# Kernel optimization log

Hardware: AMD Instinct MI355X
Metric: run time of the kernel (lower is better)

## Reference

```python
import jax, jax.numpy as jnp
import numpy as np

DIM = 128
EDGE_FEAT_DIM = 2
N_NODES = 50000
N_EDGES = 600000
EPS = 1e-5


def setup_inputs() -> dict:
    key = jax.random.key(0)
    ks = jax.random.split(key, 16)
    d = DIM
    inp = {}
    inp["x"] = jax.random.normal(ks[0], (N_NODES, d), dtype=jnp.float32)
    inp["edge_index"] = jax.random.randint(ks[1], (2, N_EDGES), 0, N_NODES, dtype=jnp.int32)
    inp["edge_weight_norm"] = jax.random.uniform(ks[2], (N_EDGES,), dtype=jnp.float32)
    inp["edge_feat"] = jax.random.normal(ks[3], (N_EDGES, EDGE_FEAT_DIM), dtype=jnp.float32)
    inp["batch"] = jnp.zeros((N_NODES,), dtype=jnp.int32)
    # phi: Linear(dim, dim)
    inp["W_phi"] = jax.random.normal(ks[4], (d, d), dtype=jnp.float32) * (1.0 / np.sqrt(d))
    inp["b_phi"] = jnp.zeros((d,), dtype=jnp.float32)
    # edge_gate: Linear(2d+2, d) -> BN(d) -> GELU -> Linear(d, 1)
    din = 2 * d + EDGE_FEAT_DIM
    inp["W_g1"] = jax.random.normal(ks[5], (din, d), dtype=jnp.float32) * (1.0 / np.sqrt(din))
    inp["b_g1"] = jnp.zeros((d,), dtype=jnp.float32)
    inp["bn_gamma"] = jnp.ones((d,), dtype=jnp.float32)
    inp["bn_beta"] = jnp.zeros((d,), dtype=jnp.float32)
    inp["bn_mean"] = jnp.zeros((d,), dtype=jnp.float32)
    inp["bn_var"] = jnp.ones((d,), dtype=jnp.float32)
    inp["W_g2"] = jax.random.normal(ks[6], (d, 1), dtype=jnp.float32) * (1.0 / np.sqrt(d))
    inp["b_g2"] = jnp.zeros((1,), dtype=jnp.float32)
    # upd: Linear(2d, d)
    inp["W_u"] = jax.random.normal(ks[7], (2 * d, d), dtype=jnp.float32) * (1.0 / np.sqrt(2 * d))
    inp["b_u"] = jnp.zeros((d,), dtype=jnp.float32)
    # LayerNorm(dim)
    inp["ln_gamma"] = jnp.ones((d,), dtype=jnp.float32)
    inp["ln_beta"] = jnp.zeros((d,), dtype=jnp.float32)
    return inp


def reference(x, edge_index, edge_weight_norm, edge_feat, batch,
              W_phi, b_phi, W_g1, b_g1, bn_gamma, bn_beta, bn_mean, bn_var,
              W_g2, b_g2, W_u, b_u, ln_gamma, ln_beta):
    src, dst = edge_index[0], edge_index[1]
    # phi(x): [N, d]
    xj = x @ W_phi + b_phi
    # edge gate MLP on [x_dst, x_src, e]: [E, 2d+2]
    g_in = jnp.concatenate([x[dst], x[src], edge_feat], axis=-1)
    h1 = g_in @ W_g1 + b_g1
    h1 = (h1 - bn_mean) * jax.lax.rsqrt(bn_var + EPS) * bn_gamma + bn_beta  # BN eval mode
    h1 = jax.nn.gelu(h1, approximate=False)
    gate = jax.nn.sigmoid(h1 @ W_g2 + b_g2)[:, 0]  # [E]
    # messages and scatter-add aggregation
    msg = xj[src] * (edge_weight_norm * gate)[:, None]  # [E, d]
    agg = jax.ops.segment_sum(msg, dst, num_segments=x.shape[0])  # [N, d]
    # update MLP + GELU + residual + LayerNorm
    h = jnp.concatenate([x, agg], axis=-1) @ W_u + b_u
    h = jax.nn.gelu(h, approximate=False)
    y = x + h
    mu = jnp.mean(y, axis=-1, keepdims=True)
    var = jnp.var(y, axis=-1, keepdims=True)
    return (y - mu) * jax.lax.rsqrt(var + EPS) * ln_gamma + ln_beta
```

## Files before the change

### kernel.cpp

```cpp
#include <hip/hip_runtime.h>
#include <hip/hip_fp16.h>
#include <math.h>

#define DIM 128
#define NN 50000
#define NE 600000
#define EPS 1e-5f
#define CAP 64

struct H8 { __half2 h[4]; };
struct F8 { float4 a, b; };

typedef _Float16 f16x8 __attribute__((ext_vector_type(8)));
typedef float    f32x4 __attribute__((ext_vector_type(4)));

__device__ __forceinline__ float gelu_fast(float x) {
    const float c1 = 2.3022085f;
    const float c2 = 0.1029437f;
    const float x2 = x * x;
    const float z  = x * __builtin_fmaf(c2, x2, c1);
    const float u  = __builtin_amdgcn_exp2f(z);
    const float r  = __builtin_amdgcn_rcpf(1.f + u);
    return __builtin_fmaf(-x, r, x);
}

__device__ __forceinline__ float sigmoid_fast(float y) {
    const float u = __builtin_amdgcn_exp2f(-1.4426950409f * y);
    return __builtin_amdgcn_rcpf(1.f + u);
}

__global__ __launch_bounds__(256) void k_prep_scale(
    const float* __restrict__ Wg1, const float* __restrict__ bg1,
    const float* __restrict__ bng, const float* __restrict__ bnb,
    const float* __restrict__ bnm, const float* __restrict__ bnv,
    __half* __restrict__ WABth, float* __restrict__ bA,
    float* __restrict__ w0p, float* __restrict__ w1p)
{
    const int k = blockIdx.x;
    const int t = threadIdx.x;
    const int c = t & 127;
    const float s = bng[c] * rsqrtf(bnv[c] + EPS);
    const float w = (t < 128) ? Wg1[k * DIM + c] : Wg1[(DIM + k) * DIM + c];
    WABth[t * DIM + k] = __float2half(w * s);
    if (k == 0 && t < 128) {
        const float tt = bnb[c] - bnm[c] * s;
        bA[c]  = bg1[c] * s + tt;
        w0p[c] = Wg1[256 * DIM + c] * s;
        w1p[c] = Wg1[257 * DIM + c] * s;
    }
}

__global__ __launch_bounds__(128) void k_prep_wpu(
    const float* __restrict__ Wphi, const float* __restrict__ bphi,
    const float* __restrict__ Wu,
    __half* __restrict__ Wct, float* __restrict__ bpu)
{
    const int a = blockIdx.x;
    const int j = threadIdx.x;
    float acc = 0.f;
    #pragma unroll 8
    for (int k = 0; k < DIM; ++k)
        acc += Wphi[a * DIM + k] * Wu[(DIM + k) * DIM + j];
    Wct[j * 256 + a]       = __float2half(Wu[a * DIM + j]);
    Wct[j * 256 + 128 + a] = __float2half(acc);
    if (a == 0) {
        float b = 0.f;
        #pragma unroll 8
        for (int k = 0; k < DIM; ++k)
            b += bphi[k] * Wu[(DIM + k) * DIM + j];
        bpu[j] = b;
    }
}

__global__ __launch_bounds__(256) void k_xh(
    const float* __restrict__ x, __half* __restrict__ xh)
{
    const int i = blockIdx.x * 256 + threadIdx.x;
    const float4 v = ((const float4*)x)[i];
    __half2 a, b;
    a.x = __float2half_rn(v.x); a.y = __float2half_rn(v.y);
    b.x = __float2half_rn(v.z); b.y = __float2half_rn(v.w);
    ((__half2*)xh)[2 * i]     = a;
    ((__half2*)xh)[2 * i + 1] = b;
}

__global__ __launch_bounds__(256) void k_node_mfma(
    const __half* __restrict__ xh, const __half* __restrict__ WABth,
    const float* __restrict__ bA,
    __half* __restrict__ A, __half* __restrict__ Bv)
{
    __shared__ __half tile[64][264];
    const int t    = threadIdx.x;
    const int wv   = t >> 6;
    const int lane = t & 63;
    const int n16  = lane & 15;
    const int quad = lane >> 4;
    const int m0   = blockIdx.x * 64;

    f32x4 acc[4][4];
    #pragma unroll
    for (int mt = 0; mt < 4; ++mt)
        #pragma unroll
        for (int nt = 0; nt < 4; ++nt)
            acc[mt][nt] = (f32x4){0.f, 0.f, 0.f, 0.f};

    int rowm[4];
    #pragma unroll
    for (int mt = 0; mt < 4; ++mt)
        rowm[mt] = min(m0 + mt * 16 + n16, NN - 1);

    #pragma unroll
    for (int ks = 0; ks < 4; ++ks) {
        const int ko = ks * 32 + quad * 8;
        f16x8 bf[4];
        #pragma unroll
        for (int nt = 0; nt < 4; ++nt) {
            const int c = wv * 64 + nt * 16 + n16;
            bf[nt] = *(const f16x8*)(WABth + c * DIM + ko);
        }
        #pragma unroll
        for (int mt = 0; mt < 4; ++mt) {
            const f16x8 af = *(const f16x8*)(xh + (size_t)rowm[mt] * DIM + ko);
            #pragma unroll
            for (int nt = 0; nt < 4; ++nt)
                acc[mt][nt] = __builtin_amdgcn_mfma_f32_16x16x32_f16(
                    af, bf[nt], acc[mt][nt], 0, 0, 0);
        }
    }

    #pragma unroll
    for (int nt = 0; nt < 4; ++nt) {
        const int c = wv * 64 + nt * 16 + n16;
        const float bias = (c < 128) ? bA[c] : 0.f;
        #pragma unroll
        for (int mt = 0; mt < 4; ++mt)
            #pragma unroll
            for (int reg = 0; reg < 4; ++reg)
                tile[mt * 16 + quad * 4 + reg][c] =
                    __float2half(acc[mt][nt][reg] + bias);
    }
    __syncthreads();

    #pragma unroll
    for (int i = 0; i < 8; ++i) {
        const int chunk = t + i * 256;
        const int row = chunk >> 5;
        const int o   = (chunk & 31) * 8;
        if (m0 + row < NN) {
            const uint4 v = *(const uint4*)&tile[row][o];
            if (o < 128) *(uint4*)(A  + (size_t)(m0 + row) * DIM + o)       = v;
            else         *(uint4*)(Bv + (size_t)(m0 + row) * DIM + o - 128) = v;
        }
    }
}

__global__ __launch_bounds__(256) void k_gate(
    const int*   __restrict__ ei,  const float* __restrict__ ew,
    const float* __restrict__ ef,
    const __half* __restrict__ A,  const __half* __restrict__ Bv,
    const float* __restrict__ w0p, const float* __restrict__ w1p,
    const float* __restrict__ Wg2, const float* __restrict__ bg2,
    int* __restrict__ deg, int2* __restrict__ pairs)
{
    const int t    = threadIdx.x;
    const int lane = t & 63;
    const int sub  = lane >> 4;
    const int sl   = lane & 15;
    const int c8   = sl * 8;
    const int e    = (blockIdx.x * 4 + (t >> 6)) * 4 + sub;

    const F8 WG = *(const F8*)(Wg2 + c8);
    const F8 W0 = *(const F8*)(w0p + c8);
    const F8 W1 = *(const F8*)(w1p + c8);
    const float bg2v = bg2[0];

    const int src = ei[e];
    const int dst = ei[NE + e];
    const float ef0 = ef[2 * e], ef1 = ef[2 * e + 1];

    const H8 av = *(const H8*)(A  + (size_t)dst * DIM + c8);
    const H8 bv = *(const H8*)(Bv + (size_t)src * DIM + c8);

    float hv[8];
    #pragma unroll
    for (int i = 0; i < 4; ++i) {
        const float2 af = __half22float2(av.h[i]);
        const float2 bf = __half22float2(bv.h[i]);
        hv[2 * i]     = af.x + bf.x;
        hv[2 * i + 1] = af.y + bf.y;
    }
    const float* w0 = (const float*)&W0;
    const float* w1 = (const float*)&W1;
    const float* wg = (const float*)&WG;
    float p = 0.f;
    #pragma unroll
    for (int i = 0; i < 8; ++i) {
        float h = hv[i] + ef0 * w0[i] + ef1 * w1[i];
        p = __builtin_fmaf(gelu_fast(h), wg[i], p);
    }
    #pragma unroll
    for (int off = 1; off < 16; off <<= 1) p += __shfl_xor(p, off, 64);

    if (sl == 0) {
        const float coef = ew[e] * sigmoid_fast(p + bg2v);
        const int pos = atomicAdd(&deg[dst], 1);
        if (pos < CAP)
            pairs[dst * CAP + pos] = make_int2(src, __float_as_int(coef));
    }
}

__global__ __launch_bounds__(256) void k_agg(
    const int* __restrict__ deg, const int2* __restrict__ pairs,
    const __half* __restrict__ xh,
    __half* __restrict__ aggh, float* __restrict__ sc)
{
    const int t    = threadIdx.x;
    const int lane = t & 63;
    const int sub  = lane >> 4;
    const int sl   = lane & 15;
    const int c8   = sl * 8;
    const int n    = blockIdx.x * 4 + (t >> 6);
    const int d    = min(deg[n], CAP);

    float acc[8];
    #pragma unroll
    for (int i = 0; i < 8; ++i) acc[i] = 0.f;
    float scn = 0.f;

    for (int j = sub; j < d; j += 4) {
        const int2 pr = pairs[n * CAP + j];
        const float cf = __int_as_float(pr.y);
        const H8 xv = *(const H8*)(xh + (size_t)pr.x * DIM + c8);
        #pragma unroll
        for (int i = 0; i < 4; ++i) {
            const float2 xf = __half22float2(xv.h[i]);
            acc[2 * i]     = __builtin_fmaf(cf, xf.x, acc[2 * i]);
            acc[2 * i + 1] = __builtin_fmaf(cf, xf.y, acc[2 * i + 1]);
        }
        scn += cf;
    }

    #pragma unroll
    for (int off = 16; off < 64; off <<= 1) {
        #pragma unroll
        for (int i = 0; i < 8; ++i) acc[i] += __shfl_xor(acc[i], off, 64);
        scn += __shfl_xor(scn, off, 64);
    }

    if (sub == 0) {
        H8 hv;
        #pragma unroll
        for (int i = 0; i < 4; ++i) {
            hv.h[i].x = __float2half_rn(acc[2 * i]);
            hv.h[i].y = __float2half_rn(acc[2 * i + 1]);
        }
        *(H8*)(aggh + (size_t)n * DIM + c8) = hv;
        if (sl == 0) sc[n] = scn;
    }
}

__global__ __launch_bounds__(256) void k_update_mfma(
    const __half* __restrict__ xh, const __half* __restrict__ aggh,
    const __half* __restrict__ Wct,
    const float* __restrict__ x,  const float* __restrict__ sc,
    const float* __restrict__ bu, const float* __restrict__ bpu,
    const float* __restrict__ lng, const float* __restrict__ lnb,
    float* __restrict__ out)
{
    const int t    = threadIdx.x;
    const int wv   = t >> 6;
    const int lane = t & 63;
    const int n16  = lane & 15;
    const int quad = lane >> 4;
    const int m0   = blockIdx.x * 64;
    const int mrow = m0 + wv * 16;
    const int arow = min(mrow + n16, NN - 1);

    f32x4 acc[8];
    #pragma unroll
    for (int nt = 0; nt < 8; ++nt) acc[nt] = (f32x4){0.f, 0.f, 0.f, 0.f};

    #pragma unroll
    for (int ks = 0; ks < 4; ++ks) {
        const int ko = ks * 32 + quad * 8;
        const f16x8 af = *(const f16x8*)(xh + (size_t)arow * DIM + ko);
        #pragma unroll
        for (int nt = 0; nt < 8; ++nt) {
            const f16x8 bf = *(const f16x8*)(Wct + (nt * 16 + n16) * 256 + ko);
            acc[nt] = __builtin_amdgcn_mfma_f32_16x16x32_f16(af, bf, acc[nt], 0, 0, 0);
        }
    }
    #pragma unroll
    for (int ks = 0; ks < 4; ++ks) {
        const int ko = ks * 32 + quad * 8;
        const f16x8 af = *(const f16x8*)(aggh + (size_t)arow * DIM + ko);
        #pragma unroll
        for (int nt = 0; nt < 8; ++nt) {
            const f16x8 bf = *(const f16x8*)(Wct + (nt * 16 + n16) * 256 + 128 + ko);
            acc[nt] = __builtin_amdgcn_mfma_f32_16x16x32_f16(af, bf, acc[nt], 0, 0, 0);
        }
    }

    int   rows[4];
    float scv[4];
    #pragma unroll
    for (int reg = 0; reg < 4; ++reg) {
        rows[reg] = mrow + quad * 4 + reg;
        scv[reg]  = sc[min(rows[reg], NN - 1)];
    }

    float yv[8][4];
    float s[4]  = {0.f, 0.f, 0.f, 0.f};
    float ss[4] = {0.f, 0.f, 0.f, 0.f};
    const float is2 = 0.70710678118654752f;

    #pragma unroll
    for (int nt = 0; nt < 8; ++nt) {
        const int c = nt * 16 + n16;
        const float buv = bu[c], bpv = bpu[c];
        #pragma unroll
        for (int reg = 0; reg < 4; ++reg) {
            float h = acc[nt][reg] + buv + scv[reg] * bpv;
            h = 0.5f * h * (1.f + erff(h * is2));
            const float xv = x[(size_t)min(rows[reg], NN - 1) * DIM + c];
            const float y = xv + h;
            yv[nt][reg] = y;
            s[reg]  += y;
            ss[reg] += y * y;
        }
    }

    #pragma unroll
    for (int reg = 0; reg < 4; ++reg) {
        #pragma unroll
        for (int off = 1; off < 16; off <<= 1) {
            s[reg]  += __shfl_xor(s[reg],  off, 64);
            ss[reg] += __shfl_xor(ss[reg], off, 64);
        }
    }

    float mu[4], rs[4];
    #pragma unroll
    for (int reg = 0; reg < 4; ++reg) {
        mu[reg] = s[reg] * (1.f / DIM);
        const float var = ss[reg] * (1.f / DIM) - mu[reg] * mu[reg];
        rs[reg] = rsqrtf(var + EPS);
    }

    #pragma unroll
    for (int nt = 0; nt < 8; ++nt) {
        const int c = nt * 16 + n16;
        const float gg = lng[c], bb = lnb[c];
        #pragma unroll
        for (int reg = 0; reg < 4; ++reg) {
            if (rows[reg] < NN)
                out[(size_t)rows[reg] * DIM + c] =
                    (yv[nt][reg] - mu[reg]) * rs[reg] * gg + bb;
        }
    }
}

extern "C" void kernel_launch(void* const* d_in, const int* in_sizes, int n_in,
                              void* d_out, int out_size, void* d_ws, size_t ws_size,
                              hipStream_t stream)
{
    const float* x    = (const float*)d_in[0];
    const int*   ei   = (const int*)  d_in[1];
    const float* ew   = (const float*)d_in[2];
    const float* ef   = (const float*)d_in[3];
    const float* Wphi = (const float*)d_in[5];
    const float* bphi = (const float*)d_in[6];
    const float* Wg1  = (const float*)d_in[7];
    const float* bg1  = (const float*)d_in[8];
    const float* bng  = (const float*)d_in[9];
    const float* bnb  = (const float*)d_in[10];
    const float* bnm  = (const float*)d_in[11];
    const float* bnv  = (const float*)d_in[12];
    const float* Wg2  = (const float*)d_in[13];
    const float* bg2  = (const float*)d_in[14];
    const float* Wu   = (const float*)d_in[15];
    const float* bu   = (const float*)d_in[16];
    const float* lng  = (const float*)d_in[17];
    const float* lnb  = (const float*)d_in[18];

    float* out = (float*)d_out;

    char* wsb = (char*)d_ws;
    size_t off = 0;
    auto carve = [&](size_t bytes) -> void* {
        void* p = wsb + off;
        off += (bytes + 255) & ~(size_t)255;
        return p;
    };
    __half* xh    = (__half*)carve((size_t)NN * DIM * 2);
    __half* A     = (__half*)carve((size_t)NN * DIM * 2);
    __half* Bv    = (__half*)carve((size_t)NN * DIM * 2);
    __half* aggh  = (__half*)carve((size_t)NN * DIM * 2);
    __half* WABth = (__half*)carve(256 * DIM * 2);
    __half* Wct   = (__half*)carve(DIM * 256 * 2);
    float*  bA    = (float*) carve(DIM * 4);
    float*  w0p   = (float*) carve(DIM * 4);
    float*  w1p   = (float*) carve(DIM * 4);
    float*  bpu   = (float*) carve(DIM * 4);
    int*    deg   = (int*)   carve((size_t)NN * 4);
    int2*   pairs = (int2*)  carve((size_t)NN * CAP * 8);
    float*  sc    = (float*) carve((size_t)NN * 4);

    hipMemsetAsync(deg, 0, (size_t)NN * 4, stream);

    k_prep_scale<<<128, 256, 0, stream>>>(Wg1, bg1, bng, bnb, bnm, bnv,
                                          WABth, bA, w0p, w1p);
    k_prep_wpu<<<128, 128, 0, stream>>>(Wphi, bphi, Wu, Wct, bpu);
    k_xh<<<(NN * DIM / 4) / 256, 256, 0, stream>>>(x, xh);
    k_node_mfma<<<(NN + 63) / 64, 256, 0, stream>>>(xh, WABth, bA, A, Bv);
    k_gate<<<NE / 16, 256, 0, stream>>>(ei, ew, ef, A, Bv, w0p, w1p, Wg2, bg2,
                                        deg, pairs);
    k_agg<<<NN / 4, 256, 0, stream>>>(deg, pairs, xh, aggh, sc);
    k_update_mfma<<<(NN + 63) / 64, 256, 0, stream>>>(xh, aggh, Wct, x, sc,
                                                      bu, bpu, lng, lnb, out);
}
```

Before: 300.7 us.

## Fuse fp16 cast into node GEMM, batch two edges per gate group, node-per-subgroup aggregation

Removes the standalone fp32-to-fp16 conversion kernel by casting x inside the node MFMA kernel, where wave 0 also writes xh. The gate kernel now handles two edges per 16-lane group using vectorized index, feature and weight loads, and adds A+B in half precision. The aggregation kernel gives each 16-lane group its own node, which drops the cross-subgroup shuffle reduction but makes per-lane work depend on node degree. The update kernel reads the residual from fp16 xh instead of fp32 x, trading some accuracy for less memory traffic.

```diff
diff --git a/kernel.cpp b/kernel.cpp
--- a/kernel.cpp
+++ b/kernel.cpp
@@ -72,22 +72,10 @@
     }
 }
 
-__global__ __launch_bounds__(256) void k_xh(
-    const float* __restrict__ x, __half* __restrict__ xh)
-{
-    const int i = blockIdx.x * 256 + threadIdx.x;
-    const float4 v = ((const float4*)x)[i];
-    __half2 a, b;
-    a.x = __float2half_rn(v.x); a.y = __float2half_rn(v.y);
-    b.x = __float2half_rn(v.z); b.y = __float2half_rn(v.w);
-    ((__half2*)xh)[2 * i]     = a;
-    ((__half2*)xh)[2 * i + 1] = b;
-}
-
 __global__ __launch_bounds__(256) void k_node_mfma(
-    const __half* __restrict__ xh, const __half* __restrict__ WABth,
+    const float* __restrict__ x, const __half* __restrict__ WABth,
     const float* __restrict__ bA,
-    __half* __restrict__ A, __half* __restrict__ Bv)
+    __half* __restrict__ A, __half* __restrict__ Bv, __half* __restrict__ xh)
 {
     __shared__ __half tile[64][264];
     const int t    = threadIdx.x;
@@ -120,7 +108,15 @@
         }
         #pragma unroll
         for (int mt = 0; mt < 4; ++mt) {
-            const f16x8 af = *(const f16x8*)(xh + (size_t)rowm[mt] * DIM + ko);
+            const float4 xa = *(const float4*)(x + (size_t)rowm[mt] * DIM + ko);
+            const float4 xb = *(const float4*)(x + (size_t)rowm[mt] * DIM + ko + 4);
+            f16x8 af;
+            af[0] = (_Float16)xa.x; af[1] = (_Float16)xa.y;
+            af[2] = (_Float16)xa.z; af[3] = (_Float16)xa.w;
+            af[4] = (_Float16)xb.x; af[5] = (_Float16)xb.y;
+            af[6] = (_Float16)xb.z; af[7] = (_Float16)xb.w;
+            if (wv == 0)
+                *(f16x8*)(xh + (size_t)rowm[mt] * DIM + ko) = af;
             #pragma unroll
             for (int nt = 0; nt < 4; ++nt)
                 acc[mt][nt] = __builtin_amdgcn_mfma_f32_16x16x32_f16(
@@ -167,45 +163,57 @@
     const int sub  = lane >> 4;
     const int sl   = lane & 15;
     const int c8   = sl * 8;
-    const int e    = (blockIdx.x * 4 + (t >> 6)) * 4 + sub;
+    const int e0   = (blockIdx.x * 4 + (t >> 6)) * 8 + sub * 2;
 
     const F8 WG = *(const F8*)(Wg2 + c8);
     const F8 W0 = *(const F8*)(w0p + c8);
     const F8 W1 = *(const F8*)(w1p + c8);
     const float bg2v = bg2[0];
-
-    const int src = ei[e];
-    const int dst = ei[NE + e];
-    const float ef0 = ef[2 * e], ef1 = ef[2 * e + 1];
-
-    const H8 av = *(const H8*)(A  + (size_t)dst * DIM + c8);
-    const H8 bv = *(const H8*)(Bv + (size_t)src * DIM + c8);
-
-    float hv[8];
-    #pragma unroll
-    for (int i = 0; i < 4; ++i) {
-        const float2 af = __half22float2(av.h[i]);
-        const float2 bf = __half22float2(bv.h[i]);
-        hv[2 * i]     = af.x + bf.x;
-        hv[2 * i + 1] = af.y + bf.y;
-    }
     const float* w0 = (const float*)&W0;
     const float* w1 = (const float*)&W1;
     const float* wg = (const float*)&WG;
-    float p = 0.f;
-    #pragma unroll
-    for (int i = 0; i < 8; ++i) {
-        float h = hv[i] + ef0 * w0[i] + ef1 * w1[i];
-        p = __builtin_fmaf(gelu_fast(h), wg[i], p);
-    }
-    #pragma unroll
-    for (int off = 1; off < 16; off <<= 1) p += __shfl_xor(p, off, 64);
+
+    const int2   srcs = *(const int2*)(ei + e0);
+    const int2   dsts = *(const int2*)(ei + NE + e0);
+    const float4 efv  = *(const float4*)(ef + 2 * e0);
+    const float2 ewv  = *(const float2*)(ew + e0);
+
+    const H8 a0 = *(const H8*)(A  + (size_t)dsts.x * DIM + c8);
+    const H8 b0 = *(const H8*)(Bv + (size_t)srcs.x * DIM + c8);
+    const H8 a1 = *(const H8*)(A  + (size_t)dsts.y * DIM + c8);
+    const H8 b1 = *(const H8*)(Bv + (size_t)srcs.y * DIM + c8);
+
+    float p0 = 0.f, p1 = 0.f;
+    #pragma unroll
+    for (int i = 0; i < 4; ++i) {
+        const float2 s0 = __half22float2(__hadd2(a0.h[i], b0.h[i]));
+        const float2 s1 = __half22float2(__hadd2(a1.h[i], b1.h[i]));
+        const int c0 = 2 * i, c1 = 2 * i + 1;
+        float h;
+        h = s0.x + efv.x * w0[c0] + efv.y * w1[c0];
+        p0 = __builtin_fmaf(gelu_fast(h), wg[c0], p0);
+        h = s0.y + efv.x * w0[c1] + efv.y * w1[c1];
+        p0 = __builtin_fmaf(gelu_fast(h), wg[c1], p0);
+        h = s1.x + efv.z * w0[c0] + efv.w * w1[c0];
+        p1 = __builtin_fmaf(gelu_fast(h), wg[c0], p1);
+        h = s1.y + efv.z * w0[c1] + efv.w * w1[c1];
+        p1 = __builtin_fmaf(gelu_fast(h), wg[c1], p1);
+    }
+    #pragma unroll
+    for (int off = 1; off < 16; off <<= 1) {
+        p0 += __shfl_xor(p0, off, 64);
+        p1 += __shfl_xor(p1, off, 64);
+    }
 
     if (sl == 0) {
-        const float coef = ew[e] * sigmoid_fast(p + bg2v);
-        const int pos = atomicAdd(&deg[dst], 1);
-        if (pos < CAP)
-            pairs[dst * CAP + pos] = make_int2(src, __float_as_int(coef));
+        const float coef0 = ewv.x * sigmoid_fast(p0 + bg2v);
+        const float coef1 = ewv.y * sigmoid_fast(p1 + bg2v);
+        const int pos0 = atomicAdd(&deg[dsts.x], 1);
+        if (pos0 < CAP)
+            pairs[(size_t)dsts.x * CAP + pos0] = make_int2(srcs.x, __float_as_int(coef0));
+        const int pos1 = atomicAdd(&deg[dsts.y], 1);
+        if (pos1 < CAP)
+            pairs[(size_t)dsts.y * CAP + pos1] = make_int2(srcs.y, __float_as_int(coef1));
     }
 }
 
@@ -219,7 +227,7 @@
     const int sub  = lane >> 4;
     const int sl   = lane & 15;
     const int c8   = sl * 8;
-    const int n    = blockIdx.x * 4 + (t >> 6);
+    const int n    = (blockIdx.x * 4 + (t >> 6)) * 4 + sub;
     const int d    = min(deg[n], CAP);
 
     float acc[8];
@@ -227,8 +235,8 @@
     for (int i = 0; i < 8; ++i) acc[i] = 0.f;
     float scn = 0.f;
 
-    for (int j = sub; j < d; j += 4) {
-        const int2 pr = pairs[n * CAP + j];
+    for (int j = 0; j < d; ++j) {
+        const int2 pr = pairs[(size_t)n * CAP + j];
         const float cf = __int_as_float(pr.y);
         const H8 xv = *(const H8*)(xh + (size_t)pr.x * DIM + c8);
         #pragma unroll
@@ -240,29 +248,20 @@
         scn += cf;
     }
 
-    #pragma unroll
-    for (int off = 16; off < 64; off <<= 1) {
-        #pragma unroll
-        for (int i = 0; i < 8; ++i) acc[i] += __shfl_xor(acc[i], off, 64);
-        scn += __shfl_xor(scn, off, 64);
-    }
-
-    if (sub == 0) {
-        H8 hv;
-        #pragma unroll
-        for (int i = 0; i < 4; ++i) {
-            hv.h[i].x = __float2half_rn(acc[2 * i]);
-            hv.h[i].y = __float2half_rn(acc[2 * i + 1]);
-        }
-        *(H8*)(aggh + (size_t)n * DIM + c8) = hv;
-        if (sl == 0) sc[n] = scn;
-    }
+    H8 hv;
+    #pragma unroll
+    for (int i = 0; i < 4; ++i) {
+        hv.h[i].x = __float2half_rn(acc[2 * i]);
+        hv.h[i].y = __float2half_rn(acc[2 * i + 1]);
+    }
+    *(H8*)(aggh + (size_t)n * DIM + c8) = hv;
+    if (sl == 0) sc[n] = scn;
 }
 
 __global__ __launch_bounds__(256) void k_update_mfma(
     const __half* __restrict__ xh, const __half* __restrict__ aggh,
     const __half* __restrict__ Wct,
-    const float* __restrict__ x,  const float* __restrict__ sc,
+    const float* __restrict__ sc,
     const float* __restrict__ bu, const float* __restrict__ bpu,
     const float* __restrict__ lng, const float* __restrict__ lnb,
     float* __restrict__ out)
@@ -322,7 +321,7 @@
         for (int reg = 0; reg < 4; ++reg) {
             float h = acc[nt][reg] + buv + scv[reg] * bpv;
             h = 0.5f * h * (1.f + erff(h * is2));
-            const float xv = x[(size_t)min(rows[reg], NN - 1) * DIM + c];
+            const float xv = __half2float(xh[(size_t)min(rows[reg], NN - 1) * DIM + c]);
             const float y = xv + h;
             yv[nt][reg] = y;
             s[reg]  += y;
@@ -411,11 +410,10 @@
     k_prep_scale<<<128, 256, 0, stream>>>(Wg1, bg1, bng, bnb, bnm, bnv,
                                           WABth, bA, w0p, w1p);
     k_prep_wpu<<<128, 128, 0, stream>>>(Wphi, bphi, Wu, Wct, bpu);
-    k_xh<<<(NN * DIM / 4) / 256, 256, 0, stream>>>(x, xh);
-    k_node_mfma<<<(NN + 63) / 64, 256, 0, stream>>>(xh, WABth, bA, A, Bv);
-    k_gate<<<NE / 16, 256, 0, stream>>>(ei, ew, ef, A, Bv, w0p, w1p, Wg2, bg2,
+    k_node_mfma<<<(NN + 63) / 64, 256, 0, stream>>>(x, WABth, bA, A, Bv, xh);
+    k_gate<<<NE / 32, 256, 0, stream>>>(ei, ew, ef, A, Bv, w0p, w1p, Wg2, bg2,
                                         deg, pairs);
-    k_agg<<<NN / 4, 256, 0, stream>>>(deg, pairs, xh, aggh, sc);
-    k_update_mfma<<<(NN + 63) / 64, 256, 0, stream>>>(xh, aggh, Wct, x, sc,
+    k_agg<<<NN / 16, 256, 0, stream>>>(deg, pairs, xh, aggh, sc);
+    k_update_mfma<<<(NN + 63) / 64, 256, 0, stream>>>(xh, aggh, Wct, sc,
                                                       bu, bpu, lng, lnb, out);
 }
```

After: 294.2 us. -2.2%, faster.
